# Optimization experiments

Hardware: AMD Instinct MI355X
Metric: run time of the kernel (lower is better)

Reference implementation:

```python
import jax, jax.numpy as jnp
import numpy as np

SRC_V, TRG_V = 36616, 23262
EMB, ENC_H, DEC_H = 300, 512, 1024
S, T, B = 50, 50, 128


def setup_inputs() -> dict:
    key = jax.random.key(0)
    ks = jax.random.split(key, 17)
    sc = 0.05
    n = lambda k, shp: (jax.random.normal(k, shp, jnp.float32) * sc)
    return {
        "input_src_batch": jax.random.randint(ks[0], (S, B), 0, SRC_V),
        "input_trg_batch": jax.random.randint(ks[1], (T, B), 0, TRG_V),
        "EEMB": n(ks[2], (SRC_V, EMB)),
        "enc_Wih_f": n(ks[3], (4 * ENC_H, EMB)),
        "enc_Whh_f": n(ks[4], (4 * ENC_H, ENC_H)),
        "enc_b_f": n(ks[5], (4 * ENC_H,)),
        "enc_Wih_r": n(ks[6], (4 * ENC_H, EMB)),
        "enc_Whh_r": n(ks[7], (4 * ENC_H, ENC_H)),
        "enc_b_r": n(ks[8], (4 * ENC_H,)),
        "attn_Wi": n(ks[9], (DEC_H, DEC_H)),
        "attn_Wo": n(ks[10], (DEC_H, 2 * DEC_H)),
        "dec_Wih": n(ks[11], (4 * DEC_H, DEC_H + EMB)),
        "dec_Whh": n(ks[12], (4 * DEC_H, DEC_H)),
        "dec_b": n(ks[13], (4 * DEC_H,)),
        "DEMB": n(ks[14], (TRG_V, EMB)),
        "gen_W": n(ks[15], (TRG_V, DEC_H)),
        "gen_b": n(ks[16], (TRG_V,)),
    }


def lstm_step(h, c, x, Wih, Whh, b):
    # PyTorch gate order: i, f, g, o
    g = x @ Wih.T + h @ Whh.T + b
    i, f, gg, o = jnp.split(g, 4, axis=-1)
    c2 = jax.nn.sigmoid(f) * c + jax.nn.sigmoid(i) * jnp.tanh(gg)
    h2 = jax.nn.sigmoid(o) * jnp.tanh(c2)
    return h2, c2


def reference(input_src_batch, input_trg_batch, EEMB, enc_Wih_f, enc_Whh_f,
              enc_b_f, enc_Wih_r, enc_Whh_r, enc_b_r, attn_Wi, attn_Wo,
              dec_Wih, dec_Whh, dec_b, DEMB, gen_W, gen_b):
    batch = input_src_batch.shape[1]
    sent_len = input_trg_batch.shape[0]
    emb = EEMB[input_src_batch]  # [S, B, 300]

    def scan_dir(xs, Wih, Whh, b):
        def f(carry, x):
            h, c = carry
            h2, c2 = lstm_step(h, c, x, Wih, Whh, b)
            return (h2, c2), h2
        init = (jnp.zeros((batch, ENC_H), emb.dtype),
                jnp.zeros((batch, ENC_H), emb.dtype))
        (hF, cF), hs = jax.lax.scan(f, init, xs)
        return hs, hF, cF

    hs_f, hF, cF = scan_dir(emb, enc_Wih_f, enc_Whh_f, enc_b_f)
    hs_r, hR, cR = scan_dir(emb[::-1], enc_Wih_r, enc_Whh_r, enc_b_r)
    hs_r = hs_r[::-1]
    enc_out = jnp.concatenate([hs_f, hs_r], axis=-1)  # [S, B, 1024]
    # torch permute(1,2,0).view(B,1024) interleaves fwd/rev per feature
    hidden = jnp.stack([hF, hR], axis=-1).reshape(batch, DEC_H)
    context = jnp.stack([cF, cR], axis=-1).reshape(batch, DEC_H)

    def attn(h):
        semi = h @ attn_Wi.T                                # [B,1024]
        score = jnp.einsum('sbd,bd->sb', enc_out, semi)     # [S,B]
        alpha = jax.nn.softmax(score, axis=0)               # softmax over src len
        s_tilde = jnp.einsum('sb,sbd->bd', alpha, enc_out)  # [B,1024]
        return jnp.tanh(jnp.concatenate([s_tilde, h], axis=1) @ attn_Wo.T)

    trg_emb = DEMB[input_trg_batch[: sent_len - 1]]  # [T-1, B, 300]

    def step(carry, x_emb):
        h, c = carry
        c_t = attn(h)
        dec_in = jnp.concatenate([c_t, x_emb], axis=1)  # [B, 1324]
        h2, c2 = lstm_step(h, c, dec_in, dec_Wih, dec_Whh, dec_b)
        logp = jax.nn.log_softmax(h2 @ gen_W.T + gen_b, axis=1)
        return (h2, c2), logp

    _, outs = jax.lax.scan(step, (hidden, context), trg_emb)  # [T-1,B,V]
    out0 = jnp.zeros((1, batch, TRG_V), outs.dtype)
    return jnp.concatenate([out0, outs], axis=0)  # [T, B, V]
```

## Files before the change

kernel.cpp:

```cpp
#include <hip/hip_runtime.h>
#include <hip/hip_bf16.h>

#define S_LEN 50
#define T_LEN 50
#define BATCH 128
#define EMB 300
#define ENC_H 512
#define DEC_H 1024
#define TRG_V 23262
#define DEC_IN (DEC_H + EMB)
#define KCAT (DEC_IN + DEC_H)
#define GN (4 * DEC_H)

static inline int cdiv(int a, int b) { return (a + b - 1) / b; }

__device__ __forceinline__ float sigm(float x) { return 1.f / (1.f + expf(-x)); }

typedef __attribute__((ext_vector_type(8))) short bf16x8;
typedef __attribute__((ext_vector_type(4))) float f32x4;

__device__ __forceinline__ void gload_lds16(const void* g, void* l) {
    __builtin_amdgcn_global_load_lds((const __attribute__((address_space(1))) int*)g,
                                     (__attribute__((address_space(3))) int*)l, 16, 0, 0);
}

__device__ __forceinline__ void gbar(unsigned* cnt, unsigned target) {
    __syncthreads();
    if (threadIdx.x == 0) {
        __threadfence();
        atomicAdd(cnt, 1u);
        while (atomicAdd(cnt, 0u) < target)
            __builtin_amdgcn_s_sleep(32);
        __threadfence();
    }
    __syncthreads();
}

__global__ __launch_bounds__(256)
void gemm_mfma_bf16(const __hip_bfloat16* __restrict__ A, const __hip_bfloat16* __restrict__ W,
                    const float* __restrict__ bias, float* __restrict__ C,
                    int M, int N, int K, int ldc)
{
    __shared__ short As[128 * 32];
    __shared__ short Bs[128 * 32];
    const int tid  = threadIdx.x;
    const int wave = tid >> 6;
    const int lane = tid & 63;
    const int m0 = blockIdx.y * 128;
    const int n0 = blockIdx.x * 128;
    const int wr = wave >> 1, wc = wave & 1;

    const int srow = lane >> 2;
    const int kgrp = lane & 3;
    const int arow0 = 32 * wave;

    f32x4 acc[4][4] = {};

    for (int k0 = 0; k0 < K; k0 += 32) {
#pragma unroll
        for (int c = 0; c < 2; c++) {
            int row = arow0 + 16 * c + srow;
            gload_lds16(A + (size_t)(m0 + row) * K + k0 + kgrp * 8,
                        &As[(arow0 + 16 * c) * 32]);
        }
#pragma unroll
        for (int c = 0; c < 2; c++) {
            int row = arow0 + 16 * c + srow;
            int gr = n0 + row; if (gr > N - 1) gr = N - 1;
            gload_lds16(W + (size_t)gr * K + k0 + kgrp * 8,
                        &Bs[(arow0 + 16 * c) * 32]);
        }
        __syncthreads();

        bf16x8 a[4], b[4];
#pragma unroll
        for (int mi = 0; mi < 4; mi++)
            a[mi] = *(const bf16x8*)&As[(wr * 64 + mi * 16 + (lane & 15)) * 32 + (lane >> 4) * 8];
#pragma unroll
        for (int ni = 0; ni < 4; ni++)
            b[ni] = *(const bf16x8*)&Bs[(wc * 64 + ni * 16 + (lane & 15)) * 32 + (lane >> 4) * 8];
#pragma unroll
        for (int mi = 0; mi < 4; mi++)
#pragma unroll
            for (int ni = 0; ni < 4; ni++)
                acc[mi][ni] = __builtin_amdgcn_mfma_f32_16x16x32_bf16(a[mi], b[ni], acc[mi][ni], 0, 0, 0);
        __syncthreads();
    }

#pragma unroll
    for (int mi = 0; mi < 4; mi++)
#pragma unroll
        for (int ni = 0; ni < 4; ni++) {
            int col = n0 + wc * 64 + ni * 16 + (lane & 15);
            if (col >= N) continue;
            float bv = bias[col];
#pragma unroll
            for (int r = 0; r < 4; r++) {
                int row = m0 + wr * 64 + mi * 16 + (lane >> 4) * 4 + r;
                C[(size_t)row * ldc + col] = acc[mi][ni][r] + bv;
            }
        }
}

__global__ void cast_f32_bf16(const float* __restrict__ in, __hip_bfloat16* __restrict__ out, size_t n)
{
    size_t i = ((size_t)blockIdx.x * blockDim.x + threadIdx.x) * 4;
    if (i + 3 < n) {
        float4 v = *(const float4*)(in + i);
        out[i + 0] = __float2bfloat16(v.x);
        out[i + 1] = __float2bfloat16(v.y);
        out[i + 2] = __float2bfloat16(v.z);
        out[i + 3] = __float2bfloat16(v.w);
    } else {
        for (; i < n; i++) out[i] = __float2bfloat16(in[i]);
    }
}

template<int BM, int BN, int BK, int TM, int TN, bool HAS_BIAS>
__global__ __launch_bounds__((BM / TM) * (BN / TN))
void gemm_bt(const float* __restrict__ A, const float* __restrict__ W,
             const float* __restrict__ bias, float* __restrict__ C,
             int M, int N, int K, int ldc)
{
    constexpr int NT  = (BM / TM) * (BN / TN);
    constexpr int NGA = TM / 4;
    constexpr int NGB = TN / 4;
    constexpr int GS  = (BN / TN) * 4;
    constexpr int LPA = BM * BK / 4 / NT;
    constexpr int LPB = BN * BK / 4 / NT;

    __shared__ float As[BK][BM + 4];
    __shared__ float Bs[BK][BN + 4];

    const int tid = threadIdx.x;
    const int tx = tid % (BN / TN);
    const int ty = tid / (BN / TN);
    const int m0 = blockIdx.y * BM;
    const int n0 = blockIdx.x * BN;

    float acc[TM][TN];
#pragma unroll
    for (int i = 0; i < TM; i++)
#pragma unroll
        for (int j = 0; j < TN; j++) acc[i][j] = 0.f;

    for (int k0 = 0; k0 < K; k0 += BK) {
#pragma unroll
        for (int e = 0; e < LPA; e++) {
            int idx = tid + e * NT;
            int r = idx / (BK / 4);
            int c4 = idx % (BK / 4);
            int row = m0 + r; if (row > M - 1) row = M - 1;
            int kk = k0 + c4 * 4;
            float4 v;
            if (kk + 3 < K) {
                v = *(const float4*)(A + (size_t)row * K + kk);
            } else {
                v.x = (kk + 0 < K) ? A[(size_t)row * K + kk + 0] : 0.f;
                v.y = (kk + 1 < K) ? A[(size_t)row * K + kk + 1] : 0.f;
                v.z = (kk + 2 < K) ? A[(size_t)row * K + kk + 2] : 0.f;
                v.w = (kk + 3 < K) ? A[(size_t)row * K + kk + 3] : 0.f;
            }
            As[c4 * 4 + 0][r] = v.x; As[c4 * 4 + 1][r] = v.y;
            As[c4 * 4 + 2][r] = v.z; As[c4 * 4 + 3][r] = v.w;
        }
#pragma unroll
        for (int e = 0; e < LPB; e++) {
            int idx = tid + e * NT;
            int r = idx / (BK / 4);
            int c4 = idx % (BK / 4);
            int row = n0 + r; if (row > N - 1) row = N - 1;
            int kk = k0 + c4 * 4;
            float4 v;
            if (kk + 3 < K) {
                v = *(const float4*)(W + (size_t)row * K + kk);
            } else {
                v.x = (kk + 0 < K) ? W[(size_t)row * K + kk + 0] : 0.f;
                v.y = (kk + 1 < K) ? W[(size_t)row * K + kk + 1] : 0.f;
                v.z = (kk + 2 < K) ? W[(size_t)row * K + kk + 2] : 0.f;
                v.w = (kk + 3 < K) ? W[(size_t)row * K + kk + 3] : 0.f;
            }
            Bs[c4 * 4 + 0][r] = v.x; Bs[c4 * 4 + 1][r] = v.y;
            Bs[c4 * 4 + 2][r] = v.z; Bs[c4 * 4 + 3][r] = v.w;
        }
        __syncthreads();
#pragma unroll
        for (int kk = 0; kk < BK; kk++) {
            float a[TM], b[TN];
#pragma unroll
            for (int g = 0; g < NGA; g++) {
                float4 v = *(const float4*)(&As[kk][ty * TM + g * 4]);
                a[g * 4 + 0] = v.x; a[g * 4 + 1] = v.y; a[g * 4 + 2] = v.z; a[g * 4 + 3] = v.w;
            }
#pragma unroll
            for (int g = 0; g < NGB; g++) {
                float4 v = *(const float4*)(&Bs[kk][tx * 4 + g * GS]);
                b[g * 4 + 0] = v.x; b[g * 4 + 1] = v.y; b[g * 4 + 2] = v.z; b[g * 4 + 3] = v.w;
            }
#pragma unroll
            for (int i = 0; i < TM; i++)
#pragma unroll
                for (int j = 0; j < TN; j++)
                    acc[i][j] = fmaf(a[i], b[j], acc[i][j]);
        }
        __syncthreads();
    }

#pragma unroll
    for (int i = 0; i < TM; i++) {
        int row = m0 + ty * TM + i;
        if (row >= M) continue;
#pragma unroll
        for (int g = 0; g < NGB; g++) {
            int colb = n0 + tx * 4 + g * GS;
#pragma unroll
            for (int j = 0; j < 4; j++) {
                int cc = colb + j;
                if (cc >= N) continue;
                float v = acc[i][g * 4 + j];
                if (HAS_BIAS) v += bias[cc];
                C[(size_t)row * ldc + cc] = v;
            }
        }
    }
}

__device__ __forceinline__ float4 g4k(const float* base, int kk, int K) {
    float4 v = make_float4(0.f, 0.f, 0.f, 0.f);
    if (kk + 3 < K) v = *(const float4*)(base + kk);
    else {
        if (kk     < K) v.x = base[kk];
        if (kk + 1 < K) v.y = base[kk + 1];
        if (kk + 2 < K) v.z = base[kk + 2];
    }
    return v;
}

__device__ __forceinline__ void tile_core(
    float (&As)[2][32][36], float (&Bs)[2][32][68],
    const float* __restrict__ A, int lda,
    const float* __restrict__ W, int ldw, int K,
    int m0, int n0, float (&acc)[2][4])
{
    const int tid = threadIdx.x;
    const int tx = tid & 15, ty = tid >> 4;
    const int ar = tid >> 3, ac4 = tid & 7;
    const float* abase = A + (size_t)(m0 + ar) * lda;
    const float* bb0   = W + (size_t)(n0 + ar) * ldw;
    const float* bb1   = bb0 + (size_t)32 * ldw;

    acc[0][0]=acc[0][1]=acc[0][2]=acc[0][3]=0.f;
    acc[1][0]=acc[1][1]=acc[1][2]=acc[1][3]=0.f;
    const int NIT = (K + 31) / 32;

    {
        int kk = ac4 * 4;
        float4 pa  = *(const float4*)(abase + kk);
        float4 pb0 = *(const float4*)(bb0 + kk);
        float4 pb1 = *(const float4*)(bb1 + kk);
        *(float4*)&As[0][ar][ac4 * 4] = pa;
        Bs[0][ac4*4+0][ar]    = pb0.x; Bs[0][ac4*4+1][ar]    = pb0.y;
        Bs[0][ac4*4+2][ar]    = pb0.z; Bs[0][ac4*4+3][ar]    = pb0.w;
        Bs[0][ac4*4+0][ar+32] = pb1.x; Bs[0][ac4*4+1][ar+32] = pb1.y;
        Bs[0][ac4*4+2][ar+32] = pb1.z; Bs[0][ac4*4+3][ar+32] = pb1.w;
    }
    __syncthreads();

    int cur = 0;
    for (int it = 0; it < NIT; ++it) {
        float4 qa, qb0, qb1;
        const bool has = (it + 1 < NIT);
        if (has) {
            int k0 = (it + 1) * 32;
            int kk = k0 + ac4 * 4;
            if (k0 + 32 <= K) { qa = *(const float4*)(abase + kk); qb0 = *(const float4*)(bb0 + kk); qb1 = *(const float4*)(bb1 + kk); }
            else { qa = g4k(abase, kk, K); qb0 = g4k(bb0, kk, K); qb1 = g4k(bb1, kk, K); }
        }
#pragma unroll
        for (int k4 = 0; k4 < 8; ++k4) {
            float4 a0 = *(const float4*)&As[cur][ty*2+0][k4*4];
            float4 a1 = *(const float4*)&As[cur][ty*2+1][k4*4];
            float4 b0 = *(const float4*)&Bs[cur][k4*4+0][tx*4];
            float4 b1 = *(const float4*)&Bs[cur][k4*4+1][tx*4];
            float4 b2 = *(const float4*)&Bs[cur][k4*4+2][tx*4];
            float4 b3 = *(const float4*)&Bs[cur][k4*4+3][tx*4];
            float av0[4] = {a0.x, a0.y, a0.z, a0.w};
            float av1[4] = {a1.x, a1.y, a1.z, a1.w};
            float4 bq[4] = {b0, b1, b2, b3};
#pragma unroll
            for (int q = 0; q < 4; q++) {
                acc[0][0] = fmaf(av0[q], bq[q].x, acc[0][0]);
                acc[0][1] = fmaf(av0[q], bq[q].y, acc[0][1]);
                acc[0][2] = fmaf(av0[q], bq[q].z, acc[0][2]);
                acc[0][3] = fmaf(av0[q], bq[q].w, acc[0][3]);
                acc[1][0] = fmaf(av1[q], bq[q].x, acc[1][0]);
                acc[1][1] = fmaf(av1[q], bq[q].y, acc[1][1]);
                acc[1][2] = fmaf(av1[q], bq[q].z, acc[1][2]);
                acc[1][3] = fmaf(av1[q], bq[q].w, acc[1][3]);
            }
        }
        if (has) {
            int nb = cur ^ 1;
            *(float4*)&As[nb][ar][ac4 * 4] = qa;
            Bs[nb][ac4*4+0][ar]    = qb0.x; Bs[nb][ac4*4+1][ar]    = qb0.y;
            Bs[nb][ac4*4+2][ar]    = qb0.z; Bs[nb][ac4*4+3][ar]    = qb0.w;
            Bs[nb][ac4*4+0][ar+32] = qb1.x; Bs[nb][ac4*4+1][ar+32] = qb1.y;
            Bs[nb][ac4*4+2][ar+32] = qb1.z; Bs[nb][ac4*4+3][ar+32] = qb1.w;
        }
        __syncthreads();
        cur ^= 1;
    }
}

__device__ __forceinline__ void attn_body(
    int b, float* hv, float* sc,
    const float* __restrict__ encP, const float* __restrict__ enc_out,
    float* __restrict__ attn_cat)
{
    const int tid = threadIdx.x;
    for (int d = tid; d < DEC_H; d += 256) hv[d] = attn_cat[(size_t)b * 2 * DEC_H + DEC_H + d];
    __syncthreads();
    int wave = tid >> 6, lane = tid & 63;
    for (int s = wave; s < S_LEN; s += 4) {
        const float* e = encP + ((size_t)s * BATCH + b) * DEC_H;
        float p = 0.f;
        for (int d = lane; d < DEC_H; d += 64) p = fmaf(e[d], hv[d], p);
        for (int off = 32; off; off >>= 1) p += __shfl_down(p, off);
        if (lane == 0) sc[s] = p;
    }
    __syncthreads();
    if (tid < 64) {
        float x = (tid < S_LEN) ? sc[tid] : -1e30f;
        float m = x;
        for (int off = 32; off; off >>= 1) m = fmaxf(m, __shfl_xor(m, off));
        float ex = (tid < S_LEN) ? expf(x - m) : 0.f;
        float ssum = ex;
        for (int off = 32; off; off >>= 1) ssum += __shfl_xor(ssum, off);
        if (tid < S_LEN) sc[tid] = ex / ssum;
    }
    __syncthreads();
    for (int d = tid; d < DEC_H; d += 256) {
        float a = 0.f;
#pragma unroll 5
        for (int s = 0; s < S_LEN; s++)
            a = fmaf(sc[s], enc_out[((size_t)s * BATCH + b) * DEC_H + d], a);
        attn_cat[(size_t)b * 2 * DEC_H + d] = a;
    }
}

__global__ __launch_bounds__(256)
void enc_persistent(const float* __restrict__ Gf, const float* __restrict__ Gr,
                    const float* __restrict__ whhF, const float* __restrict__ whhR,
                    float* __restrict__ hF2, float* __restrict__ hR2,
                    float* __restrict__ cF, float* __restrict__ cR,
                    float* __restrict__ enc_out, unsigned* __restrict__ barcnt)
{
    __shared__ struct { float As[2][32][36]; float Bs[2][32][68]; } sm;
    const int blk = blockIdx.x;
    const int tid = threadIdx.x;
    const int tx = tid & 15, ty = tid >> 4;
    const int dir = blk >> 7;
    const int id  = blk & 127;
    const int m0 = (id >> 5) * 32;
    const int n0 = (id & 31) * 64;
    const float* W  = dir ? whhR : whhF;
    float* cst      = dir ? cR : cF;
    float* hbase    = dir ? hR2 : hF2;
    const float* G  = dir ? Gr : Gf;
    const int HS = BATCH * ENC_H;
    unsigned epoch = 0;
    float acc[2][4];

    for (int t = 0; t < S_LEN; ++t) {
        const float* h_in = hbase + (size_t)(t & 1) * HS;
        float* h_out      = hbase + (size_t)((t + 1) & 1) * HS;
        int s_g = dir ? (S_LEN - 1 - t) : t;
        const float* D = G + (size_t)s_g * BATCH * 4 * ENC_H;

        tile_core(sm.As, sm.Bs, h_in, ENC_H, W, ENC_H, ENC_H, m0, n0, acc);

        int cb = n0 + tx * 4, j = cb >> 2;
#pragma unroll
        for (int i = 0; i < 2; i++) {
            int b = m0 + ty * 2 + i;
            float4 d4 = *(const float4*)(D + (size_t)b * 4 * ENC_H + cb);
            float gi = acc[i][0] + d4.x, gf = acc[i][1] + d4.y;
            float gg = acc[i][2] + d4.z, go = acc[i][3] + d4.w;
            float c2 = sigm(gf) * cst[b * ENC_H + j] + sigm(gi) * tanhf(gg);
            float h2 = sigm(go) * tanhf(c2);
            cst[b * ENC_H + j] = c2;
            h_out[b * ENC_H + j] = h2;
            enc_out[((size_t)s_g * BATCH + b) * DEC_H + dir * ENC_H + j] = h2;
        }
        if (t < S_LEN - 1) gbar(barcnt, 256u * (++epoch));
    }
}

__global__ __launch_bounds__(256)
void dec_persistent(const float* __restrict__ encP, const float* __restrict__ enc_out,
                    const int* __restrict__ trg, const float* __restrict__ DEMB,
                    const float* __restrict__ aWo, const float* __restrict__ wcat,
                    const float* __restrict__ db_i,
                    float* __restrict__ attn_cat, float* __restrict__ catA,
                    float* __restrict__ cdec, float* __restrict__ gpart,
                    __hip_bfloat16* __restrict__ H_bf, unsigned* __restrict__ barcnt)
{
    __shared__ union {
        struct { float hv[DEC_H]; float sc[S_LEN]; } a;
        struct { float As[2][32][36]; float Bs[2][32][68]; } g;
    } sm;
    const int blk = blockIdx.x;
    const int tid = threadIdx.x;
    const int tx = tid & 15, ty = tid >> 4;
    unsigned epoch = 0;
    float acc[2][4];

    for (int t = 0; t < T_LEN - 1; ++t) {
        if (blk < 128) {
            attn_body(blk, sm.a.hv, sm.a.sc, encP, enc_out, attn_cat);
        } else if (blk < 192) {
            int id = blk - 128;
            int m0 = (id >> 4) * 32, n0 = (id & 15) * 64;
            tile_core(sm.g.As, sm.g.Bs, attn_cat + DEC_H, 2 * DEC_H,
                      aWo + DEC_H, 2 * DEC_H, DEC_H, m0, n0, acc);
            int cb = n0 + tx * 4;
#pragma unroll
            for (int i = 0; i < 2; i++) {
                int row = m0 + ty * 2 + i;
                float* dst = catA + (size_t)row * KCAT + cb;
                dst[0] = acc[i][0]; dst[1] = acc[i][1];
                dst[2] = acc[i][2]; dst[3] = acc[i][3];
            }
        } else {
            int tau = blk - 192;
            int m0 = (tau >> 6) * 32, n0 = (tau & 63) * 64;
            tile_core(sm.g.As, sm.g.Bs, catA + DEC_H, KCAT,
                      wcat + DEC_H, KCAT, KCAT - DEC_H, m0, n0, acc);
            int cb = n0 + tx * 4;
#pragma unroll
            for (int i = 0; i < 2; i++) {
                int row = m0 + ty * 2 + i;
                float* dst = gpart + (size_t)row * GN + cb;
                dst[0] = acc[i][0]; dst[1] = acc[i][1];
                dst[2] = acc[i][2]; dst[3] = acc[i][3];
            }
        }
        gbar(barcnt, 256u * (++epoch));

        if (blk < 64) {
            int m0 = (blk >> 4) * 32, n0 = (blk & 15) * 64;
            tile_core(sm.g.As, sm.g.Bs, attn_cat, 2 * DEC_H, aWo, 2 * DEC_H, DEC_H, m0, n0, acc);
            int cb = n0 + tx * 4;
#pragma unroll
            for (int i = 0; i < 2; i++) {
                int row = m0 + ty * 2 + i;
                float* dst = catA + (size_t)row * KCAT + cb;
                dst[0] = tanhf(acc[i][0] + dst[0]); dst[1] = tanhf(acc[i][1] + dst[1]);
                dst[2] = tanhf(acc[i][2] + dst[2]); dst[3] = tanhf(acc[i][3] + dst[3]);
            }
        } else {
            int tau = blk;
            int m0 = (tau >> 6) * 32, n0 = (tau & 63) * 64;
            tile_core(sm.g.As, sm.g.Bs, catA + DEC_H, KCAT,
                      wcat + DEC_H, KCAT, KCAT - DEC_H, m0, n0, acc);
            int cb = n0 + tx * 4;
#pragma unroll
            for (int i = 0; i < 2; i++) {
                int row = m0 + ty * 2 + i;
                float* dst = gpart + (size_t)row * GN + cb;
                dst[0] = acc[i][0]; dst[1] = acc[i][1];
                dst[2] = acc[i][2]; dst[3] = acc[i][3];
            }
        }
        gbar(barcnt, 256u * (++epoch));

        {
            int m0 = (blk >> 6) * 32, n0 = (blk & 63) * 64;
            tile_core(sm.g.As, sm.g.Bs, catA, KCAT, wcat, KCAT, DEC_H, m0, n0, acc);
            int cb = n0 + tx * 4, j = cb >> 2;
            float4 bz = *(const float4*)(db_i + cb);
#pragma unroll
            for (int i = 0; i < 2; i++) {
                int b = m0 + ty * 2 + i;
                float4 gp = *(const float4*)(gpart + (size_t)b * GN + cb);
                float gi = acc[i][0] + gp.x + bz.x, gf = acc[i][1] + gp.y + bz.y;
                float gg = acc[i][2] + gp.z + bz.z, go = acc[i][3] + gp.w + bz.w;
                float c2 = sigm(gf) * cdec[b * DEC_H + j] + sigm(gi) * tanhf(gg);
                float h2 = sigm(go) * tanhf(c2);
                cdec[b * DEC_H + j] = c2;
                H_bf[(size_t)t * BATCH * DEC_H + b * DEC_H + j] = __float2bfloat16(h2);
                attn_cat[(size_t)b * 2 * DEC_H + DEC_H + j] = h2;
                catA[(size_t)b * KCAT + DEC_IN + j] = h2;
            }
            if ((blk & 63) == 0 && t + 1 < T_LEN - 1) {
                for (int idx = tid; idx < 32 * EMB; idx += 256) {
                    int r = m0 + idx / EMB, e = idx % EMB;
                    int idt = trg[(t + 1) * BATCH + r];
                    catA[(size_t)r * KCAT + DEC_H + e] = DEMB[(size_t)idt * EMB + e];
                }
            }
        }
        if (t < T_LEN - 2) gbar(barcnt, 256u * (++epoch));
    }
}

__global__ void zero_f32(float* p, size_t n) {
    size_t i = (size_t)blockIdx.x * blockDim.x + threadIdx.x;
    if (i < n) p[i] = 0.f;
}

__global__ void gather_rows(const int* __restrict__ ids, const float* __restrict__ E,
                            float* __restrict__ out, int nrows, int width)
{
    size_t i = (size_t)blockIdx.x * blockDim.x + threadIdx.x;
    size_t total = (size_t)nrows * width;
    if (i >= total) return;
    int r = (int)(i / width);
    int e = (int)(i % width);
    out[i] = E[(size_t)ids[r] * width + e];
}

__global__ void interleave_rows(const float* __restrict__ src, float* __restrict__ dst,
                                int units, int kdim)
{
    size_t i = (size_t)blockIdx.x * blockDim.x + threadIdx.x;
    size_t total = (size_t)4 * units * kdim;
    if (i >= total) return;
    int ir = (int)(i / kdim), k = (int)(i % kdim);
    int gate = ir & 3, j = ir >> 2;
    dst[i] = src[(size_t)(gate * units + j) * kdim + k];
}

__global__ void interleave_vec(const float* __restrict__ src, float* __restrict__ dst, int units)
{
    int i = blockIdx.x * blockDim.x + threadIdx.x;
    if (i >= 4 * units) return;
    int gate = i & 3, j = i >> 2;
    dst[i] = src[gate * units + j];
}

__global__ void build_wcat_int(const float* __restrict__ Wih, const float* __restrict__ Whh,
                               float* __restrict__ dst)
{
    size_t i = (size_t)blockIdx.x * blockDim.x + threadIdx.x;
    if (i >= (size_t)4 * DEC_H * KCAT) return;
    int ir = (int)(i / KCAT), k = (int)(i % KCAT);
    int gate = ir & 3, j = ir >> 2;
    int r = gate * DEC_H + j;
    dst[i] = (k < DEC_IN) ? Wih[(size_t)r * DEC_IN + k] : Whh[(size_t)r * DEC_H + (k - DEC_IN)];
}

__global__ void transpose_sq(const float* __restrict__ src, float* __restrict__ dst, int n)
{
    int i = blockIdx.x * blockDim.x + threadIdx.x;
    if (i >= n * n) return;
    int r = i / n, c = i % n;
    dst[(size_t)r * n + c] = src[(size_t)c * n + r];
}

__global__ void dec_init2(const float* __restrict__ hF, const float* __restrict__ cF,
                          const float* __restrict__ hR, const float* __restrict__ cR,
                          const int* __restrict__ trg, const float* __restrict__ DEMB,
                          float* __restrict__ attn_cat, float* __restrict__ catA,
                          float* __restrict__ cdec)
{
    int idx = blockIdx.x * blockDim.x + threadIdx.x;
    if (idx < BATCH * DEC_H) {
        int b = idx / DEC_H, j = idx % DEC_H;
        int half = j >> 1;
        float h = (j & 1) ? hR[b * ENC_H + half] : hF[b * ENC_H + half];
        float c = (j & 1) ? cR[b * ENC_H + half] : cF[b * ENC_H + half];
        attn_cat[(size_t)b * 2 * DEC_H + DEC_H + j] = h;
        catA[(size_t)b * KCAT + DEC_IN + j] = h;
        cdec[idx] = c;
    } else {
        int i = idx - BATCH * DEC_H;
        if (i >= BATCH * EMB) return;
        int b = i / EMB, e = i % EMB;
        catA[(size_t)b * KCAT + DEC_H + e] = DEMB[(size_t)trg[b] * EMB + e];
    }
}

__global__ __launch_bounds__(256)
void log_softmax_rows(float* __restrict__ X, int V)
{
    int row = blockIdx.x;
    float* x = X + (size_t)row * V;
    int tid = threadIdx.x;
    __shared__ float redm[4], reds[4];
    float m = -1e30f;
    for (int i = tid; i < V; i += 256) m = fmaxf(m, x[i]);
    for (int off = 32; off; off >>= 1) m = fmaxf(m, __shfl_xor(m, off));
    if ((tid & 63) == 0) redm[tid >> 6] = m;
    __syncthreads();
    m = fmaxf(fmaxf(redm[0], redm[1]), fmaxf(redm[2], redm[3]));
    float s = 0.f;
    for (int i = tid; i < V; i += 256) s += expf(x[i] - m);
    for (int off = 32; off; off >>= 1) s += __shfl_xor(s, off);
    if ((tid & 63) == 0) reds[tid >> 6] = s;
    __syncthreads();
    s = reds[0] + reds[1] + reds[2] + reds[3];
    float lg = m + logf(s);
    for (int i = tid; i < V; i += 256) x[i] -= lg;
}

static void launch_gemm_big_bias(const float* A, const float* W, const float* bias, float* C,
                                 int M, int N, int K, int ldc, hipStream_t s)
{
    dim3 g(cdiv(N, 128), cdiv(M, 128), 1);
    gemm_bt<128, 128, 16, 8, 8, true><<<g, 256, 0, s>>>(A, W, bias, C, M, N, K, ldc);
}
static void launch_gemm_big(const float* A, const float* W, float* C,
                            int M, int N, int K, int ldc, hipStream_t s)
{
    dim3 g(cdiv(N, 128), cdiv(M, 128), 1);
    gemm_bt<128, 128, 16, 8, 8, false><<<g, 256, 0, s>>>(A, W, nullptr, C, M, N, K, ldc);
}

extern "C" void kernel_launch(void* const* d_in, const int* in_sizes, int n_in,
                              void* d_out, int out_size, void* d_ws, size_t ws_size,
                              hipStream_t stream)
{
    const int*   src   = (const int*)d_in[0];
    const int*   trg   = (const int*)d_in[1];
    const float* EEMBp = (const float*)d_in[2];
    const float* eWihF = (const float*)d_in[3];
    const float* eWhhF = (const float*)d_in[4];
    const float* ebF   = (const float*)d_in[5];
    const float* eWihR = (const float*)d_in[6];
    const float* eWhhR = (const float*)d_in[7];
    const float* ebR   = (const float*)d_in[8];
    const float* aWi   = (const float*)d_in[9];
    const float* aWo   = (const float*)d_in[10];
    const float* dWih  = (const float*)d_in[11];
    const float* dWhh  = (const float*)d_in[12];
    const float* db    = (const float*)d_in[13];
    const float* DEMBp = (const float*)d_in[14];
    const float* gW    = (const float*)d_in[15];
    const float* gb    = (const float*)d_in[16];
    float* out = (float*)d_out;
    float* ws  = (float*)d_ws;

    size_t off = 0;
    auto alloc = [&](size_t n) { float* p = ws + off; off += n; return p; };

    float* Gf      = alloc((size_t)S_LEN * BATCH * 4 * ENC_H);
    float* Gr      = alloc((size_t)S_LEN * BATCH * 4 * ENC_H);
    float* emb_src = alloc((size_t)S_LEN * BATCH * EMB);
    float* enc_out = alloc((size_t)S_LEN * BATCH * DEC_H);
    float* hF2     = alloc((size_t)2 * BATCH * ENC_H);
    float* hR2     = alloc((size_t)2 * BATCH * ENC_H);
    float* cF      = alloc(BATCH * ENC_H);
    float* cR      = alloc(BATCH * ENC_H);
    float* wihF_i  = alloc((size_t)4 * ENC_H * EMB);
    float* wihR_i  = alloc((size_t)4 * ENC_H * EMB);
    float* whhF_i  = alloc((size_t)4 * ENC_H * ENC_H);
    float* whhR_i  = alloc((size_t)4 * ENC_H * ENC_H);
    float* ebF_i   = alloc(4 * ENC_H);
    float* ebR_i   = alloc(4 * ENC_H);
    float* wcat_i  = alloc((size_t)4 * DEC_H * KCAT);
    float* db_i    = alloc(4 * DEC_H);
    float* aWiT    = alloc((size_t)DEC_H * DEC_H);
    float* cdec    = alloc(BATCH * DEC_H);
    float* attn_cat= alloc((size_t)BATCH * 2 * DEC_H);
    float* catA    = alloc((size_t)BATCH * KCAT);
    float* gpart   = alloc((size_t)BATCH * GN);
    __hip_bfloat16* H_bf = (__hip_bfloat16*)alloc((size_t)(T_LEN - 1) * BATCH * DEC_H / 2);
    unsigned* barcnt = (unsigned*)alloc(16);
    __hip_bfloat16* gWb = (__hip_bfloat16*)Gf;
    float* encP = Gr;

    const int HS = BATCH * ENC_H;

    zero_f32<<<cdiv(BATCH * TRG_V, 256), 256, 0, stream>>>(out, (size_t)BATCH * TRG_V);
    zero_f32<<<cdiv(6 * HS, 256), 256, 0, stream>>>(hF2, (size_t)6 * HS);
    zero_f32<<<1, 16, 0, stream>>>((float*)barcnt, 16);

    gather_rows<<<cdiv(S_LEN * BATCH * EMB, 256), 256, 0, stream>>>(src, EEMBp, emb_src, S_LEN * BATCH, EMB);

    interleave_rows<<<cdiv(4 * ENC_H * EMB, 256), 256, 0, stream>>>(eWihF, wihF_i, ENC_H, EMB);
    interleave_rows<<<cdiv(4 * ENC_H * EMB, 256), 256, 0, stream>>>(eWihR, wihR_i, ENC_H, EMB);
    interleave_rows<<<cdiv(4 * ENC_H * ENC_H, 256), 256, 0, stream>>>(eWhhF, whhF_i, ENC_H, ENC_H);
    interleave_rows<<<cdiv(4 * ENC_H * ENC_H, 256), 256, 0, stream>>>(eWhhR, whhR_i, ENC_H, ENC_H);
    interleave_vec<<<cdiv(4 * ENC_H, 256), 256, 0, stream>>>(ebF, ebF_i, ENC_H);
    interleave_vec<<<cdiv(4 * ENC_H, 256), 256, 0, stream>>>(ebR, ebR_i, ENC_H);
    build_wcat_int<<<cdiv(4 * DEC_H * KCAT, 256), 256, 0, stream>>>(dWih, dWhh, wcat_i);
    interleave_vec<<<cdiv(4 * DEC_H, 256), 256, 0, stream>>>(db, db_i, DEC_H);
    transpose_sq<<<cdiv(DEC_H * DEC_H, 256), 256, 0, stream>>>(aWi, aWiT, DEC_H);

    launch_gemm_big_bias(emb_src, wihF_i, ebF_i, Gf, S_LEN * BATCH, 4 * ENC_H, EMB, 4 * ENC_H, stream);
    launch_gemm_big_bias(emb_src, wihR_i, ebR_i, Gr, S_LEN * BATCH, 4 * ENC_H, EMB, 4 * ENC_H, stream);

    enc_persistent<<<256, 256, 0, stream>>>(Gf, Gr, whhF_i, whhR_i, hF2, hR2, cF, cR,
                                            enc_out, &barcnt[0]);

    launch_gemm_big(enc_out, aWiT, encP, S_LEN * BATCH, DEC_H, DEC_H, DEC_H, stream);

    cast_f32_bf16<<<cdiv((int)((size_t)TRG_V * DEC_H / 4), 256), 256, 0, stream>>>(gW, gWb, (size_t)TRG_V * DEC_H);

    dec_init2<<<cdiv(BATCH * DEC_H + BATCH * EMB, 256), 256, 0, stream>>>(
        hF2, cF, hR2, cR, trg, DEMBp, attn_cat, catA, cdec);

    dec_persistent<<<256, 256, 0, stream>>>(encP, enc_out, trg, DEMBp, aWo, wcat_i, db_i,
                                            attn_cat, catA, cdec, gpart, H_bf, &barcnt[1]);

    {
        dim3 g(cdiv(TRG_V, 128), cdiv((T_LEN - 1) * BATCH, 128), 1);
        gemm_mfma_bf16<<<g, 256, 0, stream>>>(H_bf, gWb, gb, out + (size_t)BATCH * TRG_V,
                                              (T_LEN - 1) * BATCH, TRG_V, DEC_H, TRG_V);
    }

    log_softmax_rows<<<(T_LEN - 1) * BATCH, 256, 0, stream>>>(out + (size_t)BATCH * TRG_V, TRG_V);
}
```

Measured before the change: 14.17 ms.

## Drop grid-barrier fences, use agent-scope relaxed atomics for cross-block data

Removes the __threadfence calls around the persistent-kernel grid barrier. Every cross-block shared buffer (hidden state, catA, gpart, attn_cat) is now read and written through relaxed agent-scope atomic loads and stores, so visibility comes from coherent accesses instead of full fences. The tiled SGEMM core also gains a two-stage register prefetch that loads two tiles ahead. Relaxed atomics with no fences rely on ordering by the barrier atomics, which risks memory-ordering bugs, and the atomic accesses may be split into narrower transactions.

```diff
diff --git a/kernel.cpp b/kernel.cpp
--- a/kernel.cpp
+++ b/kernel.cpp
@@ -24,14 +24,35 @@
                                      (__attribute__((address_space(3))) int*)l, 16, 0, 0);
 }
 
+__device__ __forceinline__ float cload1(const float* p) {
+    return __hip_atomic_load(p, __ATOMIC_RELAXED, __HIP_MEMORY_SCOPE_AGENT);
+}
+__device__ __forceinline__ float2 cload2(const float* p) {
+    unsigned long long u = __hip_atomic_load((const unsigned long long*)p,
+                                             __ATOMIC_RELAXED, __HIP_MEMORY_SCOPE_AGENT);
+    union U { unsigned long long u; float2 f; } c; c.u = u; return c.f;
+}
+__device__ __forceinline__ float4 cload4(const float* p) {
+    float2 a = cload2(p), b = cload2(p + 2);
+    return make_float4(a.x, a.y, b.x, b.y);
+}
+__device__ __forceinline__ void cstore1(float* p, float v) {
+    __hip_atomic_store(p, v, __ATOMIC_RELAXED, __HIP_MEMORY_SCOPE_AGENT);
+}
+__device__ __forceinline__ void cstore2(float* p, float2 v) {
+    union U { unsigned long long u; float2 f; } c; c.f = v;
+    __hip_atomic_store((unsigned long long*)p, c.u, __ATOMIC_RELAXED, __HIP_MEMORY_SCOPE_AGENT);
+}
+__device__ __forceinline__ void cstore4(float* p, float4 v) {
+    cstore2(p, make_float2(v.x, v.y)); cstore2(p + 2, make_float2(v.z, v.w));
+}
+
 __device__ __forceinline__ void gbar(unsigned* cnt, unsigned target) {
     __syncthreads();
     if (threadIdx.x == 0) {
-        __threadfence();
         atomicAdd(cnt, 1u);
         while (atomicAdd(cnt, 0u) < target)
             __builtin_amdgcn_s_sleep(32);
-        __threadfence();
     }
     __syncthreads();
 }
@@ -235,6 +256,16 @@
     }
     return v;
 }
+__device__ __forceinline__ float4 g4kc(const float* base, int kk, int K) {
+    float4 v = make_float4(0.f, 0.f, 0.f, 0.f);
+    if (kk + 3 < K) v = cload4(base + kk);
+    else {
+        if (kk     < K) v.x = cload1(base + kk);
+        if (kk + 1 < K) v.y = cload1(base + kk + 1);
+        if (kk + 2 < K) v.z = cload1(base + kk + 2);
+    }
+    return v;
+}
 
 __device__ __forceinline__ void tile_core(
     float (&As)[2][32][36], float (&Bs)[2][32][68],
@@ -253,37 +284,33 @@
     acc[1][0]=acc[1][1]=acc[1][2]=acc[1][3]=0.f;
     const int NIT = (K + 31) / 32;
 
-    {
-        int kk = ac4 * 4;
-        float4 pa  = *(const float4*)(abase + kk);
-        float4 pb0 = *(const float4*)(bb0 + kk);
-        float4 pb1 = *(const float4*)(bb1 + kk);
-        *(float4*)&As[0][ar][ac4 * 4] = pa;
-        Bs[0][ac4*4+0][ar]    = pb0.x; Bs[0][ac4*4+1][ar]    = pb0.y;
-        Bs[0][ac4*4+2][ar]    = pb0.z; Bs[0][ac4*4+3][ar]    = pb0.w;
-        Bs[0][ac4*4+0][ar+32] = pb1.x; Bs[0][ac4*4+1][ar+32] = pb1.y;
-        Bs[0][ac4*4+2][ar+32] = pb1.z; Bs[0][ac4*4+3][ar+32] = pb1.w;
-    }
-    __syncthreads();
-
-    int cur = 0;
-    for (int it = 0; it < NIT; ++it) {
-        float4 qa, qb0, qb1;
-        const bool has = (it + 1 < NIT);
-        if (has) {
-            int k0 = (it + 1) * 32;
-            int kk = k0 + ac4 * 4;
-            if (k0 + 32 <= K) { qa = *(const float4*)(abase + kk); qb0 = *(const float4*)(bb0 + kk); qb1 = *(const float4*)(bb1 + kk); }
-            else { qa = g4k(abase, kk, K); qb0 = g4k(bb0, kk, K); qb1 = g4k(bb1, kk, K); }
-        }
+    float4 pa0, pb00, pb10;
+    float4 pa1, pb01, pb11;
+
+    auto LOAD = [&](int itx, float4& qa, float4& qb0, float4& qb1) {
+        int k0 = itx * 32, kk = k0 + ac4 * 4;
+        if (k0 + 32 <= K) {
+            qa = cload4(abase + kk); qb0 = *(const float4*)(bb0 + kk); qb1 = *(const float4*)(bb1 + kk);
+        } else {
+            qa = g4kc(abase, kk, K); qb0 = g4k(bb0, kk, K); qb1 = g4k(bb1, kk, K);
+        }
+    };
+    auto SLDS = [&](int nb, const float4& qa, const float4& qb0, const float4& qb1) {
+        *(float4*)&As[nb][ar][ac4 * 4] = qa;
+        Bs[nb][ac4*4+0][ar]    = qb0.x; Bs[nb][ac4*4+1][ar]    = qb0.y;
+        Bs[nb][ac4*4+2][ar]    = qb0.z; Bs[nb][ac4*4+3][ar]    = qb0.w;
+        Bs[nb][ac4*4+0][ar+32] = qb1.x; Bs[nb][ac4*4+1][ar+32] = qb1.y;
+        Bs[nb][ac4*4+2][ar+32] = qb1.z; Bs[nb][ac4*4+3][ar+32] = qb1.w;
+    };
+    auto COMP = [&](int c) {
 #pragma unroll
         for (int k4 = 0; k4 < 8; ++k4) {
-            float4 a0 = *(const float4*)&As[cur][ty*2+0][k4*4];
-            float4 a1 = *(const float4*)&As[cur][ty*2+1][k4*4];
-            float4 b0 = *(const float4*)&Bs[cur][k4*4+0][tx*4];
-            float4 b1 = *(const float4*)&Bs[cur][k4*4+1][tx*4];
-            float4 b2 = *(const float4*)&Bs[cur][k4*4+2][tx*4];
-            float4 b3 = *(const float4*)&Bs[cur][k4*4+3][tx*4];
+            float4 a0 = *(const float4*)&As[c][ty*2+0][k4*4];
+            float4 a1 = *(const float4*)&As[c][ty*2+1][k4*4];
+            float4 b0 = *(const float4*)&Bs[c][k4*4+0][tx*4];
+            float4 b1 = *(const float4*)&Bs[c][k4*4+1][tx*4];
+            float4 b2 = *(const float4*)&Bs[c][k4*4+2][tx*4];
+            float4 b3 = *(const float4*)&Bs[c][k4*4+3][tx*4];
             float av0[4] = {a0.x, a0.y, a0.z, a0.w};
             float av1[4] = {a1.x, a1.y, a1.z, a1.w};
             float4 bq[4] = {b0, b1, b2, b3};
@@ -299,16 +326,27 @@
                 acc[1][3] = fmaf(av1[q], bq[q].w, acc[1][3]);
             }
         }
-        if (has) {
-            int nb = cur ^ 1;
-            *(float4*)&As[nb][ar][ac4 * 4] = qa;
-            Bs[nb][ac4*4+0][ar]    = qb0.x; Bs[nb][ac4*4+1][ar]    = qb0.y;
-            Bs[nb][ac4*4+2][ar]    = qb0.z; Bs[nb][ac4*4+3][ar]    = qb0.w;
-            Bs[nb][ac4*4+0][ar+32] = qb1.x; Bs[nb][ac4*4+1][ar+32] = qb1.y;
-            Bs[nb][ac4*4+2][ar+32] = qb1.z; Bs[nb][ac4*4+3][ar+32] = qb1.w;
-        }
+    };
+
+    LOAD(0, pa0, pb00, pb10);
+    if (NIT > 1) LOAD(1, pa1, pb01, pb11);
+    SLDS(0, pa0, pb00, pb10);
+    __syncthreads();
+
+    int cur = 0;
+    int it = 0;
+    while (it < NIT) {
+        if (it + 2 < NIT) LOAD(it + 2, pa0, pb00, pb10);
+        COMP(cur);
+        if (it + 1 < NIT) SLDS(cur ^ 1, pa1, pb01, pb11);
         __syncthreads();
-        cur ^= 1;
+        cur ^= 1; ++it;
+        if (it >= NIT) break;
+        if (it + 2 < NIT) LOAD(it + 2, pa1, pb01, pb11);
+        COMP(cur);
+        if (it + 1 < NIT) SLDS(cur ^ 1, pa0, pb00, pb10);
+        __syncthreads();
+        cur ^= 1; ++it;
     }
 }
 
@@ -318,7 +356,7 @@
     float* __restrict__ attn_cat)
 {
     const int tid = threadIdx.x;
-    for (int d = tid; d < DEC_H; d += 256) hv[d] = attn_cat[(size_t)b * 2 * DEC_H + DEC_H + d];
+    for (int d = tid; d < DEC_H; d += 256) hv[d] = cload1(&attn_cat[(size_t)b * 2 * DEC_H + DEC_H + d]);
     __syncthreads();
     int wave = tid >> 6, lane = tid & 63;
     for (int s = wave; s < S_LEN; s += 4) {
@@ -344,7 +382,7 @@
 #pragma unroll 5
         for (int s = 0; s < S_LEN; s++)
             a = fmaf(sc[s], enc_out[((size_t)s * BATCH + b) * DEC_H + d], a);
-        attn_cat[(size_t)b * 2 * DEC_H + d] = a;
+        cstore1(&attn_cat[(size_t)b * 2 * DEC_H + d], a);
     }
 }
 
@@ -389,7 +427,7 @@
             float c2 = sigm(gf) * cst[b * ENC_H + j] + sigm(gi) * tanhf(gg);
             float h2 = sigm(go) * tanhf(c2);
             cst[b * ENC_H + j] = c2;
-            h_out[b * ENC_H + j] = h2;
+            cstore1(&h_out[b * ENC_H + j], h2);
             enc_out[((size_t)s_g * BATCH + b) * DEC_H + dir * ENC_H + j] = h2;
         }
         if (t < S_LEN - 1) gbar(barcnt, 256u * (++epoch));
@@ -427,9 +465,8 @@
 #pragma unroll
             for (int i = 0; i < 2; i++) {
                 int row = m0 + ty * 2 + i;
-                float* dst = catA + (size_t)row * KCAT + cb;
-                dst[0] = acc[i][0]; dst[1] = acc[i][1];
-                dst[2] = acc[i][2]; dst[3] = acc[i][3];
+                cstore4(catA + (size_t)row * KCAT + cb,
+                        make_float4(acc[i][0], acc[i][1], acc[i][2], acc[i][3]));
             }
         } else {
             int tau = blk - 192;
@@ -440,9 +477,8 @@
 #pragma unroll
             for (int i = 0; i < 2; i++) {
                 int row = m0 + ty * 2 + i;
-                float* dst = gpart + (size_t)row * GN + cb;
-                dst[0] = acc[i][0]; dst[1] = acc[i][1];
-                dst[2] = acc[i][2]; dst[3] = acc[i][3];
+                cstore4(gpart + (size_t)row * GN + cb,
+                        make_float4(acc[i][0], acc[i][1], acc[i][2], acc[i][3]));
             }
         }
         gbar(barcnt, 256u * (++epoch));
@@ -455,8 +491,9 @@
             for (int i = 0; i < 2; i++) {
                 int row = m0 + ty * 2 + i;
                 float* dst = catA + (size_t)row * KCAT + cb;
-                dst[0] = tanhf(acc[i][0] + dst[0]); dst[1] = tanhf(acc[i][1] + dst[1]);
-                dst[2] = tanhf(acc[i][2] + dst[2]); dst[3] = tanhf(acc[i][3] + dst[3]);
+                float4 prev = cload4(dst);
+                cstore4(dst, make_float4(tanhf(acc[i][0] + prev.x), tanhf(acc[i][1] + prev.y),
+                                         tanhf(acc[i][2] + prev.z), tanhf(acc[i][3] + prev.w)));
             }
         } else {
             int tau = blk;
@@ -467,9 +504,8 @@
 #pragma unroll
             for (int i = 0; i < 2; i++) {
                 int row = m0 + ty * 2 + i;
-                float* dst = gpart + (size_t)row * GN + cb;
-                dst[0] = acc[i][0]; dst[1] = acc[i][1];
-                dst[2] = acc[i][2]; dst[3] = acc[i][3];
+                cstore4(gpart + (size_t)row * GN + cb,
+                        make_float4(acc[i][0], acc[i][1], acc[i][2], acc[i][3]));
             }
         }
         gbar(barcnt, 256u * (++epoch));
@@ -482,21 +518,21 @@
 #pragma unroll
             for (int i = 0; i < 2; i++) {
                 int b = m0 + ty * 2 + i;
-                float4 gp = *(const float4*)(gpart + (size_t)b * GN + cb);
+                float4 gp = cload4(gpart + (size_t)b * GN + cb);
                 float gi = acc[i][0] + gp.x + bz.x, gf = acc[i][1] + gp.y + bz.y;
                 float gg = acc[i][2] + gp.z + bz.z, go = acc[i][3] + gp.w + bz.w;
                 float c2 = sigm(gf) * cdec[b * DEC_H + j] + sigm(gi) * tanhf(gg);
                 float h2 = sigm(go) * tanhf(c2);
                 cdec[b * DEC_H + j] = c2;
                 H_bf[(size_t)t * BATCH * DEC_H + b * DEC_H + j] = __float2bfloat16(h2);
-                attn_cat[(size_t)b * 2 * DEC_H + DEC_H + j] = h2;
-                catA[(size_t)b * KCAT + DEC_IN + j] = h2;
+                cstore1(&attn_cat[(size_t)b * 2 * DEC_H + DEC_H + j], h2);
+                cstore1(&catA[(size_t)b * KCAT + DEC_IN + j], h2);
             }
             if ((blk & 63) == 0 && t + 1 < T_LEN - 1) {
                 for (int idx = tid; idx < 32 * EMB; idx += 256) {
                     int r = m0 + idx / EMB, e = idx % EMB;
                     int idt = trg[(t + 1) * BATCH + r];
-                    catA[(size_t)r * KCAT + DEC_H + e] = DEMB[(size_t)idt * EMB + e];
+                    cstore1(&catA[(size_t)r * KCAT + DEC_H + e], DEMB[(size_t)idt * EMB + e]);
                 }
             }
         }
```

Measured after the change: 12.52 ms. 11.6% less time.
